# Performance work log

Hardware: AMD Instinct MI355X
Metric: run time of the kernel (lower is better)

Reference implementation:

```python
import jax, jax.numpy as jnp
import numpy as np

BATCH = 65536
IN_FEATURES = 128
OUT_FEATURES = 128
GRID = 8  # initial_grid: number of RBF/spline basis centers per edge


def setup_inputs() -> dict:
    key = jax.random.key(0)
    k1, k2, k3 = jax.random.split(key, 3)
    x = jax.random.normal(k1, (BATCH, IN_FEATURES), dtype=jnp.float32)
    # Per-edge spline coefficients stacked: [out, in, grid]
    coeffs = jax.random.normal(k2, (OUT_FEATURES, IN_FEATURES, GRID), dtype=jnp.float32) * 0.1
    # Per-edge base (SiLU) weights stacked: [out, in]
    base_w = jax.random.normal(k3, (OUT_FEATURES, IN_FEATURES), dtype=jnp.float32) * 0.1
    # Shared uniform grid of RBF centers in [-1, 1]
    centers = jnp.linspace(-1.0, 1.0, GRID, dtype=jnp.float32)
    return {"x": x, "coeffs": coeffs, "base_w": base_w, "centers": centers}


def reference(x, coeffs, base_w, centers):
    # HybridBasisFunction per edge: base_w * silu(x) + sum_g coeffs[g] * exp(-((x-c_g)/w)^2)
    width = 2.0 / (GRID - 1)  # grid spacing
    # basis: [B, in, G]
    diff = (x[:, :, None] - centers[None, None, :]) / width
    basis = jnp.exp(-diff * diff)
    # Sum over all edges (j -> i): output[b, i] = sum_j phi_ij(x[b, j])
    out = jnp.einsum('big,oig->bo', basis, coeffs)
    out = out + jnp.einsum('bi,oi->bo', jax.nn.silu(x), base_w)
    return out
```

## Files before the change

### kernel.cpp

```cpp
#include <hip/hip_runtime.h>

typedef __fp16   pk16x2 __attribute__((ext_vector_type(2)));
typedef _Float16 f16x8  __attribute__((ext_vector_type(8)));
typedef float    f32x4  __attribute__((ext_vector_type(4)));
typedef float    f32x16 __attribute__((ext_vector_type(16)));

#define BATCH 65536
#define NIN   128
#define NOUT  128

#define L2E   1.4426950408889634f
#define SQL2E 1.2011224087864498f
#define EM2   0.1353352832366127f


__global__ __launch_bounds__(256) void kan_prep(const float* __restrict__ coeffs,
                                                const float* __restrict__ base_w,
                                                _Float16* __restrict__ W3) {
    int t = blockIdx.x * 256 + threadIdx.x;
    int ks   = t >> 8;
    int c    = t & 255;
    int nbb  = c >> 6;
    int lane = c & 63;
    int sub  = lane >> 5;
    int col  = nbb * 32 + (lane & 31);
    f16x8 v;
    if (ks < 64) {
        int g = ks >> 3, t2 = ks & 7;
        const float* src = coeffs + ((size_t)col * 128 + g * 16 + sub * 8 + t2) * 8;
#pragma unroll
        for (int e = 0; e < 8; ++e) v[e] = (_Float16)src[e];
    } else {
        const float* src = base_w + (size_t)col * 128 + (ks - 64) * 16 + sub * 8;
#pragma unroll
        for (int e = 0; e < 8; ++e) v[e] = (_Float16)src[e];
    }
    *(f16x8*)((char*)W3 + (size_t)t * 16) = v;
}

__device__ __forceinline__ void gll16(const void* g, void* l) {
    __builtin_amdgcn_global_load_lds(
        (const __attribute__((address_space(1))) unsigned int*)g,
        (__attribute__((address_space(3))) unsigned int*)l, 16, 0, 0);
}

__device__ __forceinline__ f16x8 basis8r(float t) {
    float u  = t * SQL2E;
    float b0 = __builtin_amdgcn_exp2f(-(u * u));
    float r  = __builtin_amdgcn_exp2f(__builtin_fmaf(t, 2.0f * L2E, -L2E));
    float b1 = b0 * r; r *= EM2;
    float b2 = b1 * r; r *= EM2;
    float b3 = b2 * r; r *= EM2;
    float b4 = b3 * r; r *= EM2;
    float b5 = b4 * r; r *= EM2;
    float b6 = b5 * r; r *= EM2;
    float b7 = b6 * r;
    pk16x2 p0 = __builtin_amdgcn_cvt_pkrtz(b0, b1);
    pk16x2 p1 = __builtin_amdgcn_cvt_pkrtz(b2, b3);
    pk16x2 p2 = __builtin_amdgcn_cvt_pkrtz(b4, b5);
    pk16x2 p3 = __builtin_amdgcn_cvt_pkrtz(b6, b7);
    f16x8 o;
    o[0] = p0[0]; o[1] = p0[1]; o[2] = p1[0]; o[3] = p1[1];
    o[4] = p2[0]; o[5] = p2[1]; o[6] = p3[0]; o[7] = p3[1];
    return o;
}

__device__ __forceinline__ float silu1(float xv) {
    float p = __builtin_amdgcn_exp2f(-xv * L2E);
    return xv * __builtin_amdgcn_rcpf(1.0f + p);
}

__global__ __launch_bounds__(256, 2) void kan_main(const float* __restrict__ x,
                                                   const _Float16* __restrict__ W3,
                                                   float* __restrict__ out) {
    __shared__ _Float16 smem[2][16384];

    const int tid   = threadIdx.x;
    const int lane  = tid & 63;
    const int w     = tid >> 6;
    const int l31   = lane & 31;
    const int sub   = lane >> 5;
    const int row0  = blockIdx.x * 128 + w * 32;
    const int start = blockIdx.x & 7;

    const float* xp = x + (size_t)(row0 + l31) * NIN;

    f32x16 acc[4];
#pragma unroll
    for (int nbb = 0; nbb < 4; ++nbb)
#pragma unroll
        for (int r = 0; r < 16; ++r) acc[nbb][r] = 0.f;

    const char* wbase = (const char*)W3;
#define STAGE(buf, grp)                                                         \
    do {                                                                        \
        const char* _s = wbase + (size_t)(grp) * 32768 + (size_t)tid * 16;      \
        char*       _d = (char*)&smem[(buf)][0] + (size_t)tid * 16;             \
        _Pragma("unroll")                                                       \
        for (int _i = 0; _i < 8; ++_i) gll16(_s + _i * 4096, _d + _i * 4096);   \
    } while (0)

    STAGE(0, start);
    f32x4 xa = *(const f32x4*)(xp + start * 16 + sub * 8);
    f32x4 xb = *(const f32x4*)(xp + start * 16 + sub * 8 + 4);
    __syncthreads();

#pragma unroll
    for (int i = 0; i < 8; ++i) {
        const int cur = i & 1;
        const int nxtg = (i < 7) ? ((start + i + 1) & 7) : 8;
        STAGE(cur ^ 1, nxtg);
        const int nxt = (i < 7) ? (((start + i + 1) & 7) * 16) : 0;
        f32x4 xa2 = *(const f32x4*)(xp + nxt + sub * 8);
        f32x4 xb2 = *(const f32x4*)(xp + nxt + sub * 8 + 4);

        f16x8 a[8];
#pragma unroll
        for (int t2 = 0; t2 < 4; ++t2) a[t2]     = basis8r(__builtin_fmaf(xa[t2], 3.5f, 3.5f));
#pragma unroll
        for (int t2 = 0; t2 < 4; ++t2) a[4 + t2] = basis8r(__builtin_fmaf(xb[t2], 3.5f, 3.5f));

        __builtin_amdgcn_s_setprio(1);
#pragma unroll
        for (int t2 = 0; t2 < 8; ++t2) {
            const char* bp = (const char*)&smem[cur][0] + t2 * 4096 + lane * 16;
#pragma unroll
            for (int nbb = 0; nbb < 4; ++nbb) {
                f16x8 b = *(const f16x8*)(bp + nbb * 1024);
                acc[nbb] = __builtin_amdgcn_mfma_f32_32x32x16_f16(a[t2], b, acc[nbb], 0, 0, 0);
            }
        }
        __builtin_amdgcn_s_setprio(0);
        xa = xa2; xb = xb2;
        __syncthreads();
    }

#pragma unroll
    for (int s = 0; s < 8; ++s) {
        f32x4 xa2, xb2;
        if (s < 7) {
            xa2 = *(const f32x4*)(xp + (s + 1) * 16 + sub * 8);
            xb2 = *(const f32x4*)(xp + (s + 1) * 16 + sub * 8 + 4);
        }
        float s0 = silu1(xa[0]), s1 = silu1(xa[1]), s2 = silu1(xa[2]), s3 = silu1(xa[3]);
        float s4 = silu1(xb[0]), s5 = silu1(xb[1]), s6 = silu1(xb[2]), s7 = silu1(xb[3]);
        pk16x2 p0 = __builtin_amdgcn_cvt_pkrtz(s0, s1);
        pk16x2 p1 = __builtin_amdgcn_cvt_pkrtz(s2, s3);
        pk16x2 p2 = __builtin_amdgcn_cvt_pkrtz(s4, s5);
        pk16x2 p3 = __builtin_amdgcn_cvt_pkrtz(s6, s7);
        f16x8 a;
        a[0] = p0[0]; a[1] = p0[1]; a[2] = p1[0]; a[3] = p1[1];
        a[4] = p2[0]; a[5] = p2[1]; a[6] = p3[0]; a[7] = p3[1];
        const char* bp = (const char*)&smem[0][0] + s * 4096 + lane * 16;
        __builtin_amdgcn_s_setprio(1);
#pragma unroll
        for (int nbb = 0; nbb < 4; ++nbb) {
            f16x8 b = *(const f16x8*)(bp + nbb * 1024);
            acc[nbb] = __builtin_amdgcn_mfma_f32_32x32x16_f16(a, b, acc[nbb], 0, 0, 0);
        }
        __builtin_amdgcn_s_setprio(0);
        if (s < 7) { xa = xa2; xb = xb2; }
    }

#pragma unroll
    for (int nbb = 0; nbb < 4; ++nbb)
#pragma unroll
        for (int r = 0; r < 16; ++r) {
            int crow = (r & 3) + 8 * (r >> 2) + 4 * sub;
            out[(size_t)(row0 + crow) * NOUT + nbb * 32 + l31] = acc[nbb][r];
        }
}

extern "C" void kernel_launch(void* const* d_in, const int* in_sizes, int n_in,
                              void* d_out, int out_size, void* d_ws, size_t ws_size,
                              hipStream_t stream) {
    const float* x       = (const float*)d_in[0];
    const float* coeffs  = (const float*)d_in[1];
    const float* base_w  = (const float*)d_in[2];
    _Float16* W3 = (_Float16*)d_ws;

    kan_prep<<<dim3(72), dim3(256), 0, stream>>>(coeffs, base_w, W3);
    kan_main<<<dim3(BATCH / 128), dim3(256), 0, stream>>>(x, W3, (float*)d_out);
}
```

Before: 37.17 us.

## Software-pipeline basis compute and LDS loads with MFMAs, stagger block start

Restructures the spline inner loop so the LDS fragment for the next k-step and the basis for step t2+2 are issued while the current step's MFMAs run. The intent is to interleave VALU exp work and LDS reads with matrix ops instead of computing all basis values first. It also removes the s_setprio calls, packs fp16 halves via a bitcast to u32x4 to avoid element shuffles, and makes some blocks sleep briefly at start to desynchronize their phases. These add register pressure under launch_bounds(256,2) and a small startup delay for some blocks.

```diff
diff --git a/kernel.cpp b/kernel.cpp
--- a/kernel.cpp
+++ b/kernel.cpp
@@ -1,9 +1,10 @@
 #include <hip/hip_runtime.h>
 
-typedef __fp16   pk16x2 __attribute__((ext_vector_type(2)));
-typedef _Float16 f16x8  __attribute__((ext_vector_type(8)));
-typedef float    f32x4  __attribute__((ext_vector_type(4)));
-typedef float    f32x16 __attribute__((ext_vector_type(16)));
+typedef __fp16       pk16x2 __attribute__((ext_vector_type(2)));
+typedef _Float16     f16x8  __attribute__((ext_vector_type(8)));
+typedef float        f32x4  __attribute__((ext_vector_type(4)));
+typedef float        f32x16 __attribute__((ext_vector_type(16)));
+typedef unsigned int u32x4  __attribute__((ext_vector_type(4)));
 
 #define BATCH 65536
 #define NIN   128
@@ -55,14 +56,12 @@
     float b5 = b4 * r; r *= EM2;
     float b6 = b5 * r; r *= EM2;
     float b7 = b6 * r;
-    pk16x2 p0 = __builtin_amdgcn_cvt_pkrtz(b0, b1);
-    pk16x2 p1 = __builtin_amdgcn_cvt_pkrtz(b2, b3);
-    pk16x2 p2 = __builtin_amdgcn_cvt_pkrtz(b4, b5);
-    pk16x2 p3 = __builtin_amdgcn_cvt_pkrtz(b6, b7);
-    f16x8 o;
-    o[0] = p0[0]; o[1] = p0[1]; o[2] = p1[0]; o[3] = p1[1];
-    o[4] = p2[0]; o[5] = p2[1]; o[6] = p3[0]; o[7] = p3[1];
-    return o;
+    u32x4 U;
+    U[0] = __builtin_bit_cast(unsigned int, __builtin_amdgcn_cvt_pkrtz(b0, b1));
+    U[1] = __builtin_bit_cast(unsigned int, __builtin_amdgcn_cvt_pkrtz(b2, b3));
+    U[2] = __builtin_bit_cast(unsigned int, __builtin_amdgcn_cvt_pkrtz(b4, b5));
+    U[3] = __builtin_bit_cast(unsigned int, __builtin_amdgcn_cvt_pkrtz(b6, b7));
+    return __builtin_bit_cast(f16x8, U);
 }
 
 __device__ __forceinline__ float silu1(float xv) {
@@ -82,6 +81,10 @@
     const int sub   = lane >> 5;
     const int row0  = blockIdx.x * 128 + w * 32;
     const int start = blockIdx.x & 7;
+
+    const int slp = (blockIdx.x & 1) + ((blockIdx.x >> 8) & 1);
+    if (slp > 0) __builtin_amdgcn_s_sleep(10);
+    if (slp > 1) __builtin_amdgcn_s_sleep(10);
 
     const float* xp = x + (size_t)(row0 + l31) * NIN;
 
@@ -107,30 +110,42 @@
 
 #pragma unroll
     for (int i = 0; i < 8; ++i) {
-        const int cur = i & 1;
+        const int cur  = i & 1;
         const int nxtg = (i < 7) ? ((start + i + 1) & 7) : 8;
         STAGE(cur ^ 1, nxtg);
         const int nxt = (i < 7) ? (((start + i + 1) & 7) * 16) : 0;
         f32x4 xa2 = *(const f32x4*)(xp + nxt + sub * 8);
         f32x4 xb2 = *(const f32x4*)(xp + nxt + sub * 8 + 4);
 
+        const char* bpbase = (const char*)&smem[cur][0] + lane * 16;
+
         f16x8 a[8];
+        a[0] = basis8r(__builtin_fmaf(xa[0], 3.5f, 3.5f));
+        a[1] = basis8r(__builtin_fmaf(xa[1], 3.5f, 3.5f));
+        f16x8 b[4];
 #pragma unroll
-        for (int t2 = 0; t2 < 4; ++t2) a[t2]     = basis8r(__builtin_fmaf(xa[t2], 3.5f, 3.5f));
-#pragma unroll
-        for (int t2 = 0; t2 < 4; ++t2) a[4 + t2] = basis8r(__builtin_fmaf(xb[t2], 3.5f, 3.5f));
+        for (int q = 0; q < 4; ++q) b[q] = *(const f16x8*)(bpbase + q * 1024);
 
-        __builtin_amdgcn_s_setprio(1);
 #pragma unroll
         for (int t2 = 0; t2 < 8; ++t2) {
-            const char* bp = (const char*)&smem[cur][0] + t2 * 4096 + lane * 16;
+            f16x8 bn[4];
+            if (t2 < 7) {
 #pragma unroll
-            for (int nbb = 0; nbb < 4; ++nbb) {
-                f16x8 b = *(const f16x8*)(bp + nbb * 1024);
-                acc[nbb] = __builtin_amdgcn_mfma_f32_32x32x16_f16(a[t2], b, acc[nbb], 0, 0, 0);
+                for (int q = 0; q < 4; ++q)
+                    bn[q] = *(const f16x8*)(bpbase + (t2 + 1) * 4096 + q * 1024);
+            }
+            if (t2 < 6) {
+                float xs = (t2 + 2 < 4) ? xa[t2 + 2] : xb[(t2 + 2) & 3];
+                a[t2 + 2] = basis8r(__builtin_fmaf(xs, 3.5f, 3.5f));
+            }
+#pragma unroll
+            for (int q = 0; q < 4; ++q)
+                acc[q] = __builtin_amdgcn_mfma_f32_32x32x16_f16(a[t2], b[q], acc[q], 0, 0, 0);
+            if (t2 < 7) {
+#pragma unroll
+                for (int q = 0; q < 4; ++q) b[q] = bn[q];
             }
         }
-        __builtin_amdgcn_s_setprio(0);
         xa = xa2; xb = xb2;
         __syncthreads();
     }
@@ -142,32 +157,31 @@
             xa2 = *(const f32x4*)(xp + (s + 1) * 16 + sub * 8);
             xb2 = *(const f32x4*)(xp + (s + 1) * 16 + sub * 8 + 4);
         }
-        float s0 = silu1(xa[0]), s1 = silu1(xa[1]), s2 = silu1(xa[2]), s3 = silu1(xa[3]);
-        float s4 = silu1(xb[0]), s5 = silu1(xb[1]), s6 = silu1(xb[2]), s7 = silu1(xb[3]);
-        pk16x2 p0 = __builtin_amdgcn_cvt_pkrtz(s0, s1);
-        pk16x2 p1 = __builtin_amdgcn_cvt_pkrtz(s2, s3);
-        pk16x2 p2 = __builtin_amdgcn_cvt_pkrtz(s4, s5);
-        pk16x2 p3 = __builtin_amdgcn_cvt_pkrtz(s6, s7);
-        f16x8 a;
-        a[0] = p0[0]; a[1] = p0[1]; a[2] = p1[0]; a[3] = p1[1];
-        a[4] = p2[0]; a[5] = p2[1]; a[6] = p3[0]; a[7] = p3[1];
+        u32x4 U;
+        U[0] = __builtin_bit_cast(unsigned int,
+               __builtin_amdgcn_cvt_pkrtz(silu1(xa[0]), silu1(xa[1])));
+        U[1] = __builtin_bit_cast(unsigned int,
+               __builtin_amdgcn_cvt_pkrtz(silu1(xa[2]), silu1(xa[3])));
+        U[2] = __builtin_bit_cast(unsigned int,
+               __builtin_amdgcn_cvt_pkrtz(silu1(xb[0]), silu1(xb[1])));
+        U[3] = __builtin_bit_cast(unsigned int,
+               __builtin_amdgcn_cvt_pkrtz(silu1(xb[2]), silu1(xb[3])));
+        f16x8 a = __builtin_bit_cast(f16x8, U);
         const char* bp = (const char*)&smem[0][0] + s * 4096 + lane * 16;
-        __builtin_amdgcn_s_setprio(1);
 #pragma unroll
-        for (int nbb = 0; nbb < 4; ++nbb) {
-            f16x8 b = *(const f16x8*)(bp + nbb * 1024);
-            acc[nbb] = __builtin_amdgcn_mfma_f32_32x32x16_f16(a, b, acc[nbb], 0, 0, 0);
+        for (int q = 0; q < 4; ++q) {
+            f16x8 bq = *(const f16x8*)(bp + q * 1024);
+            acc[q] = __builtin_amdgcn_mfma_f32_32x32x16_f16(a, bq, acc[q], 0, 0, 0);
         }
-        __builtin_amdgcn_s_setprio(0);
         if (s < 7) { xa = xa2; xb = xb2; }
     }
 
 #pragma unroll
-    for (int nbb = 0; nbb < 4; ++nbb)
+    for (int q = 0; q < 4; ++q)
 #pragma unroll
         for (int r = 0; r < 16; ++r) {
             int crow = (r & 3) + 8 * (r >> 2) + 4 * sub;
-            out[(size_t)(row0 + crow) * NOUT + nbb * 32 + l31] = acc[nbb][r];
+            out[(size_t)(row0 + crow) * NOUT + q * 32 + l31] = acc[q][r];
         }
 }
 
```

Result: slower. 39.87 us (+7.3%).
